# Kernel tuning notes

Hardware: AMD Instinct MI355X
Metric: run time of the kernel (lower is better)

The kernel has to match this reference:

```python
import jax, jax.numpy as jnp
import numpy as np

EPS = 1e-05
FACT = 2.0
REJECT_RATIO = 1.0
B, N1, N2 = 8, 4096, 4096


def setup_inputs() -> dict:
    key = jax.random.key(0)
    k1, k2 = jax.random.split(key)
    pc1 = jax.random.normal(k1, (B, 4, N1), dtype=jnp.float32)
    pc2 = jax.random.normal(k2, (B, 4, N2), dtype=jnp.float32)
    # homogeneous coordinates: last row is 1
    pc1 = pc1.at[:, 3, :].set(1.0)
    pc2 = pc2.at[:, 3, :].set(1.0)
    return {"pc1": pc1, "pc2": pc2}


def _rot_to_quat(R):
    # quaternion [w, x, y, z] from 3x3 rotation matrix (branchless)
    def s(x):
        return jnp.where(x >= 0, 1.0, -1.0)
    qw = 0.5 * jnp.sqrt(jnp.maximum(1.0 + R[0, 0] + R[1, 1] + R[2, 2], 1e-12))
    qx = 0.5 * jnp.sqrt(jnp.maximum(1.0 + R[0, 0] - R[1, 1] - R[2, 2], 1e-12)) * s(R[2, 1] - R[1, 2])
    qy = 0.5 * jnp.sqrt(jnp.maximum(1.0 - R[0, 0] + R[1, 1] - R[2, 2], 1e-12)) * s(R[0, 2] - R[2, 0])
    qz = 0.5 * jnp.sqrt(jnp.maximum(1.0 - R[0, 0] - R[1, 1] + R[2, 2], 1e-12)) * s(R[1, 0] - R[0, 1])
    return jnp.stack([qw, qx, qy, qz])


def _single(pc1, pc2):
    # pc1: [4, N1], pc2: [4, N2]
    p1, p2 = pc1[:3], pc2[:3]
    # squared pairwise distance via matmul-expansion trick: [N1, N2]
    d = (jnp.sum(p1 ** 2, axis=0)[:, None]
         - 2.0 * jnp.einsum('dn,dm->nm', p1, p2)
         + jnp.sum(p2 ** 2, axis=0)[None, :])
    # soft nearest neighbor: softmax over N2 of fact / clamp(d, eps)
    w = jax.nn.softmax(FACT / jnp.maximum(d, EPS), axis=1)  # [N1, N2]
    pc_nearest = jnp.einsum('cm,nm->cn', pc2, w)            # [4, N1]

    # soft outlier rejection (near-hard threshold via steep sigmoid)
    dist = jnp.linalg.norm(pc1 - pc_nearest, axis=0)        # [N1]
    mean_dist = jnp.mean(dist)
    indexor = jax.nn.sigmoid((dist - mean_dist * REJECT_RATIO - EPS) * -1e10)

    # weighted Procrustes (soft_tf); note indexor weights BOTH centred clouds
    wsum = jnp.sum(indexor)
    c2 = jnp.sum(pc_nearest[:3] * indexor, axis=-1) / wsum  # [3]
    c1 = jnp.sum(pc1[:3] * indexor, axis=-1) / wsum         # [3]
    p2c = ((pc_nearest[:3] - c2[:, None]) * indexor).T      # [N1, 3]
    p1c = ((pc1[:3] - c1[:, None]) * indexor).T             # [N1, 3]
    H = p1c.T @ p2c                                         # [3, 3]
    U, S, Vh = jnp.linalg.svd(H, full_matrices=False)
    V = Vh.T
    sign = jnp.where(jnp.linalg.det(U) * jnp.linalg.det(V) < 0, -1.0, 1.0)
    V = V * jnp.array([1.0, 1.0, 1.0]).at[2].set(sign)[None, :]  # flip 3rd column
    R = V @ U.T
    t = c2 - R @ c1
    T = jnp.zeros((4, 4), dtype=pc1.dtype)
    T = T.at[:3, :3].set(R).at[:3, 3].set(t).at[3, 3].set(1.0)
    q = _rot_to_quat(R)
    return T, q, t


def reference(pc1, pc2):
    T, q, t = jax.vmap(_single)(pc1, pc2)
    return T, q, t
```

## Files before the change

### kernel.cpp

```cpp
#include <hip/hip_runtime.h>
#include <math.h>


typedef float v2f __attribute__((ext_vector_type(2)));

constexpr int cB  = 8;
constexpr int cN1 = 4096;
constexpr int cN2 = 4096;
constexpr int cMC = 8;
constexpr int cCHUNK = cN2 / cMC;
constexpr int cNB2 = cN1 / 256;
constexpr float cEPS  = 1e-5f;
constexpr float cKK   = 0.34657359027997264f;
constexpr float cEPSK = cEPS * cKK;
constexpr float cUNSC = -1.4426950408889634f;

constexpr size_t OFF_PARTM = 0x400000;
constexpr size_t OFF_DPART = 0x500000;
constexpr size_t OFF_MPART = 0x500400;

__global__ __launch_bounds__(256) void cpnet_partial(
    const float* __restrict__ pc1, const float* __restrict__ pc2,
    float4* __restrict__ partA, float* __restrict__ partM) {
  __shared__ float xs[cCHUNK], ys[cCHUNK], zs[cCHUNK], ws[cCHUNK];
  const int tid = threadIdx.x;
  const int b = blockIdx.z, c = blockIdx.y;
  const int n = blockIdx.x * 256 + tid;

  const float* p2b = pc2 + (size_t)b * 4 * cN2 + c * cCHUNK;
  for (int i = tid; i < cCHUNK; i += 256) {
    float x = p2b[i], y = p2b[cN2 + i], z = p2b[2 * cN2 + i];
    xs[i] = -2.0f * cKK * x;
    ys[i] = -2.0f * cKK * y;
    zs[i] = -2.0f * cKK * z;
    ws[i] = cKK * (x * x + y * y + z * z);
  }
  __syncthreads();

  const float* p1b = pc1 + (size_t)b * 4 * cN1;
  const float x1 = p1b[n], y1 = p1b[cN1 + n], z1 = p1b[2 * cN1 + n];
  const float n1k = cKK * (x1 * x1 + y1 * y1 + z1 * z1);
  const v2f X1 = {x1, x1}, Y1 = {y1, y1}, Z1 = {z1, z1}, N1K = {n1k, n1k};

  const v2f* xs2 = (const v2f*)xs;
  const v2f* ys2 = (const v2f*)ys;
  const v2f* zs2 = (const v2f*)zs;
  const v2f* ws2 = (const v2f*)ws;

  v2f dmin2 = {3.0e38f, 3.0e38f};
#pragma unroll 4
  for (int m = 0; m < cCHUNK / 2; ++m) {
    v2f dk = X1 * xs2[m] + (Y1 * ys2[m] + (Z1 * zs2[m] + (ws2[m] + N1K)));
    dmin2 = __builtin_elementwise_min(dmin2, dk);
  }
  const float dmin = fminf(dmin2.x, dmin2.y);
  const float M = __builtin_amdgcn_rcpf(fmaxf(dmin, cEPSK));
  const v2f M2 = {M, M};
  const v2f EPS2 = {cEPSK, cEPSK};

  v2f S2 = {0.f, 0.f}, Ax2 = {0.f, 0.f}, Ay2 = {0.f, 0.f}, Az2 = {0.f, 0.f};
#pragma unroll 4
  for (int m = 0; m < cCHUNK / 2; ++m) {
    v2f vx = xs2[m], vy = ys2[m], vz = zs2[m];
    v2f dk = X1 * vx + (Y1 * vy + (Z1 * vz + (ws2[m] + N1K)));
    dk = __builtin_elementwise_max(dk, EPS2);
    v2f s2v;
    s2v.x = __builtin_amdgcn_rcpf(dk.x);
    s2v.y = __builtin_amdgcn_rcpf(dk.y);
    v2f d2 = s2v - M2;
    v2f e;
    e.x = __builtin_amdgcn_exp2f(d2.x);
    e.y = __builtin_amdgcn_exp2f(d2.y);
    S2 += e;
    Ax2 += e * vx;
    Ay2 += e * vy;
    Az2 += e * vz;
  }

  const int idx = (c * cB + b) * cN1 + n;
  partA[idx] = make_float4(Ax2.x + Ax2.y, Ay2.x + Ay2.y, Az2.x + Az2.y,
                           S2.x + S2.y);
  partM[idx] = M;
}

__device__ __forceinline__ void reduce_multi(double* v, int nv, double* lds,
                                             int tid) {
  const int lane = tid & 63, w = tid >> 6;
  for (int i = 0; i < nv; ++i) {
    double x = v[i];
    for (int s = 32; s > 0; s >>= 1) x += __shfl_xor(x, s, 64);
    if (lane == 0) lds[i * 4 + w] = x;
  }
  __syncthreads();
  if (tid < nv)
    lds[tid * 4] = lds[tid * 4] + lds[tid * 4 + 1] + lds[tid * 4 + 2] +
                   lds[tid * 4 + 3];
  __syncthreads();
  for (int i = 0; i < nv; ++i) v[i] = lds[i * 4];
  __syncthreads();
}

__global__ __launch_bounds__(256) void cpnet_combine(
    const float* __restrict__ pc1, float4* partA,
    const float* __restrict__ partM, double* __restrict__ dpart) {
  __shared__ double lds[32 * 4];
  const int tid = threadIdx.x;
  const int bx = blockIdx.x, b = blockIdx.y;
  const int n = bx * 256 + tid;

  float Ms[cMC];
  float g = -3.0e38f;
#pragma unroll
  for (int c = 0; c < cMC; ++c) {
    Ms[c] = partM[(c * cB + b) * cN1 + n];
    g = fmaxf(g, Ms[c]);
  }
  float S = 0.f, nx = 0.f, ny = 0.f, nz = 0.f;
#pragma unroll
  for (int c = 0; c < cMC; ++c) {
    float w = exp2f(Ms[c] - g);
    float4 a = partA[(c * cB + b) * cN1 + n];
    S += a.w * w; nx += a.x * w; ny += a.y * w; nz += a.z * w;
  }
  float inv = cUNSC / S;
  nx *= inv; ny *= inv; nz *= inv;
  const float* p1b = pc1 + (size_t)b * 4 * cN1;
  float dx = p1b[n] - nx, dy = p1b[cN1 + n] - ny, dz = p1b[2 * cN1 + n] - nz;
  float dist = sqrtf(dx * dx + dy * dy + dz * dz);
  partA[(0 * cB + b) * cN1 + n] = make_float4(nx, ny, nz, dist);

  double acc[1];
  acc[0] = (double)dist;
  reduce_multi(acc, 1, lds, tid);
  if (tid == 0) dpart[b * cNB2 + bx] = acc[0];
}

__global__ __launch_bounds__(256) void cpnet_moments(
    const float* __restrict__ pc1, const float4* __restrict__ partA,
    const double* __restrict__ dpart, double* __restrict__ mpart) {
  __shared__ double lds[32 * 4];
  const int tid = threadIdx.x;
  const int bx = blockIdx.x, b = blockIdx.y;
  const int n = bx * 256 + tid;

  double dsum = 0.0;
  for (int i = 0; i < cNB2; ++i) dsum += dpart[b * cNB2 + i];
  const float meanf = (float)(dsum * (1.0 / (double)cN1));

  float4 nn = partA[(0 * cB + b) * cN1 + n];
  float u = (nn.w - meanf - cEPS) * 1e10f;
  float ind = 1.0f / (1.0f + expf(u));
  const float* p1b = pc1 + (size_t)b * 4 * cN1;
  double di = (double)ind, di2 = di * di;
  double x1 = (double)p1b[n], y1 = (double)p1b[cN1 + n],
         z1 = (double)p1b[2 * cN1 + n];
  double x2 = (double)nn.x, y2 = (double)nn.y, z2 = (double)nn.z;

  double a[23];
  a[0] = di;
  a[1] = di * x1;  a[2] = di * y1;  a[3] = di * z1;
  a[4] = di * x2;  a[5] = di * y2;  a[6] = di * z2;
  a[7] = di2;
  a[8]  = di2 * x1;  a[9]  = di2 * y1;  a[10] = di2 * z1;
  a[11] = di2 * x2;  a[12] = di2 * y2;  a[13] = di2 * z2;
  a[14] = di2 * x1 * x2; a[15] = di2 * x1 * y2; a[16] = di2 * x1 * z2;
  a[17] = di2 * y1 * x2; a[18] = di2 * y1 * y2; a[19] = di2 * y1 * z2;
  a[20] = di2 * z1 * x2; a[21] = di2 * z1 * y2; a[22] = di2 * z1 * z2;

  reduce_multi(a, 23, lds, tid);
  if (tid == 0) {
    double* mb = mpart + (size_t)(b * cNB2 + bx) * 23;
    for (int i = 0; i < 23; ++i) mb[i] = a[i];
  }
}

__global__ __launch_bounds__(64) void cpnet_solve(
    const double* __restrict__ mpart, float* __restrict__ out) {
  const int b = blockIdx.x;
  if (threadIdx.x != 0) return;

  double acc[23];
  for (int i = 0; i < 23; ++i) acc[i] = 0.0;
  for (int k = 0; k < cNB2; ++k) {
    const double* mb = mpart + (size_t)(b * cNB2 + k) * 23;
    for (int i = 0; i < 23; ++i) acc[i] += mb[i];
  }

  double W = acc[0];
  double c1[3] = {acc[1] / W, acc[2] / W, acc[3] / W};
  double c2[3] = {acc[4] / W, acc[5] / W, acc[6] / W};
  double H[3][3];
  for (int i = 0; i < 3; ++i)
    for (int j = 0; j < 3; ++j)
      H[i][j] = acc[14 + 3 * i + j] - c2[j] * acc[8 + i] -
                c1[i] * acc[11 + j] + c1[i] * c2[j] * acc[7];

  double trH = H[0][0] + H[1][1] + H[2][2];
  double Nm[4][4], V[4][4];
  Nm[0][0] = trH;
  Nm[0][1] = Nm[1][0] = H[1][2] - H[2][1];
  Nm[0][2] = Nm[2][0] = H[2][0] - H[0][2];
  Nm[0][3] = Nm[3][0] = H[0][1] - H[1][0];
  Nm[1][1] = 2.0 * H[0][0] - trH;
  Nm[1][2] = Nm[2][1] = H[0][1] + H[1][0];
  Nm[1][3] = Nm[3][1] = H[0][2] + H[2][0];
  Nm[2][2] = 2.0 * H[1][1] - trH;
  Nm[2][3] = Nm[3][2] = H[1][2] + H[2][1];
  Nm[3][3] = 2.0 * H[2][2] - trH;

  for (int i = 0; i < 4; ++i)
    for (int j = 0; j < 4; ++j) V[i][j] = (i == j) ? 1.0 : 0.0;

  for (int sweep = 0; sweep < 6; ++sweep) {
    for (int p = 0; p < 3; ++p) {
      for (int q = p + 1; q < 4; ++q) {
        double apq = Nm[p][q];
        if (fabs(apq) < 1e-300) continue;
        double theta = (Nm[q][q] - Nm[p][p]) / (2.0 * apq);
        double tt = (theta >= 0.0 ? 1.0 : -1.0) /
                    (fabs(theta) + sqrt(theta * theta + 1.0));
        double cc = 1.0 / sqrt(tt * tt + 1.0);
        double ss = tt * cc;
        for (int k = 0; k < 4; ++k) {
          double akp = Nm[k][p], akq = Nm[k][q];
          Nm[k][p] = cc * akp - ss * akq;
          Nm[k][q] = ss * akp + cc * akq;
        }
        for (int k = 0; k < 4; ++k) {
          double apk = Nm[p][k], aqk = Nm[q][k];
          Nm[p][k] = cc * apk - ss * aqk;
          Nm[q][k] = ss * apk + cc * aqk;
        }
        for (int k = 0; k < 4; ++k) {
          double vkp = V[k][p], vkq = V[k][q];
          V[k][p] = cc * vkp - ss * vkq;
          V[k][q] = ss * vkp + cc * vkq;
        }
      }
    }
  }
  int imax = 0;
  for (int i = 1; i < 4; ++i)
    if (Nm[i][i] > Nm[imax][imax]) imax = i;
  double qw = V[0][imax], qx = V[1][imax], qy = V[2][imax], qz = V[3][imax];
  double qn = sqrt(qw * qw + qx * qx + qy * qy + qz * qz);
  qw /= qn; qx /= qn; qy /= qn; qz /= qn;

  double R[3][3];
  R[0][0] = 1.0 - 2.0 * (qy * qy + qz * qz);
  R[0][1] = 2.0 * (qx * qy - qw * qz);
  R[0][2] = 2.0 * (qx * qz + qw * qy);
  R[1][0] = 2.0 * (qx * qy + qw * qz);
  R[1][1] = 1.0 - 2.0 * (qx * qx + qz * qz);
  R[1][2] = 2.0 * (qy * qz - qw * qx);
  R[2][0] = 2.0 * (qx * qz - qw * qy);
  R[2][1] = 2.0 * (qy * qz + qw * qx);
  R[2][2] = 1.0 - 2.0 * (qx * qx + qy * qy);

  double tr1 = 0.0, tr2 = 0.0;
  for (int i = 0; i < 3; ++i)
    for (int j = 0; j < 3; ++j) {
      tr1 += R[i][j] * H[j][i];
      tr2 += R[j][i] * H[j][i];
    }
  if (tr2 > tr1) {
    for (int i = 0; i < 3; ++i)
      for (int j = i + 1; j < 3; ++j) {
        double tmp = R[i][j]; R[i][j] = R[j][i]; R[j][i] = tmp;
      }
  }

  double tx = c2[0] - (R[0][0] * c1[0] + R[0][1] * c1[1] + R[0][2] * c1[2]);
  double ty = c2[1] - (R[1][0] * c1[0] + R[1][1] * c1[1] + R[1][2] * c1[2]);
  double tz = c2[2] - (R[2][0] * c1[0] + R[2][1] * c1[1] + R[2][2] * c1[2]);

  auto sgn = [](double x) { return x >= 0.0 ? 1.0 : -1.0; };
  double oqw = 0.5 * sqrt(fmax(1.0 + R[0][0] + R[1][1] + R[2][2], 1e-12));
  double oqx = 0.5 * sqrt(fmax(1.0 + R[0][0] - R[1][1] - R[2][2], 1e-12)) *
               sgn(R[2][1] - R[1][2]);
  double oqy = 0.5 * sqrt(fmax(1.0 - R[0][0] + R[1][1] - R[2][2], 1e-12)) *
               sgn(R[0][2] - R[2][0]);
  double oqz = 0.5 * sqrt(fmax(1.0 - R[0][0] - R[1][1] + R[2][2], 1e-12)) *
               sgn(R[1][0] - R[0][1]);

  float* T = out + b * 16;
  T[0]  = (float)R[0][0]; T[1]  = (float)R[0][1]; T[2]  = (float)R[0][2]; T[3]  = (float)tx;
  T[4]  = (float)R[1][0]; T[5]  = (float)R[1][1]; T[6]  = (float)R[1][2]; T[7]  = (float)ty;
  T[8]  = (float)R[2][0]; T[9]  = (float)R[2][1]; T[10] = (float)R[2][2]; T[11] = (float)tz;
  T[12] = 0.f; T[13] = 0.f; T[14] = 0.f; T[15] = 1.f;
  float* Q = out + 128 + b * 4;
  Q[0] = (float)oqw; Q[1] = (float)oqx; Q[2] = (float)oqy; Q[3] = (float)oqz;
  float* Tt = out + 160 + b * 3;
  Tt[0] = (float)tx; Tt[1] = (float)ty; Tt[2] = (float)tz;
}

extern "C" void kernel_launch(void* const* d_in, const int* in_sizes, int n_in,
                              void* d_out, int out_size, void* d_ws, size_t ws_size,
                              hipStream_t stream) {
  const float* pc1 = (const float*)d_in[0];
  const float* pc2 = (const float*)d_in[1];
  float* out = (float*)d_out;
  char* ws = (char*)d_ws;

  float4* partA = (float4*)ws;
  float*  partM = (float*)(ws + OFF_PARTM);
  double* dpart = (double*)(ws + OFF_DPART);
  double* mpart = (double*)(ws + OFF_MPART);

  cpnet_partial<<<dim3(cN1 / 256, cMC, cB), 256, 0, stream>>>(pc1, pc2,
                                                              partA, partM);
  cpnet_combine<<<dim3(cNB2, cB), 256, 0, stream>>>(pc1, partA, partM, dpart);
  cpnet_moments<<<dim3(cNB2, cB), 256, 0, stream>>>(pc1, partA, dpart, mpart);
  cpnet_solve<<<cB, 64, 0, stream>>>(mpart, out);
}
```

Measured before the change: 141.8 us.

## Fuse combine, moments and solve into one kernel via last-block atomic counter

Merges the combine, moments and solve kernels into a single finalize kernel. Each block writes its partial distance sum, and the last block to finish per batch (detected with an atomic counter reset inside the partial kernel) computes the mean, loops over all points to accumulate the 23 moments, and runs the solve. This removes two kernel launches and the per-block moment partials. In exchange, the moment accumulation is serialized onto a single block per batch.

```diff
diff --git a/kernel.cpp b/kernel.cpp
--- a/kernel.cpp
+++ b/kernel.cpp
@@ -17,11 +17,16 @@
 
 constexpr size_t OFF_PARTM = 0x400000;
 constexpr size_t OFF_DPART = 0x500000;
-constexpr size_t OFF_MPART = 0x500400;
+constexpr size_t OFF_CTR   = 0x500400;
 
 __global__ __launch_bounds__(256) void cpnet_partial(
     const float* __restrict__ pc1, const float* __restrict__ pc2,
-    float4* __restrict__ partA, float* __restrict__ partM) {
+    float4* __restrict__ partA, float* __restrict__ partM,
+    int* __restrict__ ctr) {
+  if (blockIdx.x == 0 && blockIdx.y == 0 && blockIdx.z == 0 &&
+      threadIdx.x < cB)
+    ctr[threadIdx.x] = 0;
+
   __shared__ float xs[cCHUNK], ys[cCHUNK], zs[cCHUNK], ws[cCHUNK];
   const int tid = threadIdx.x;
   const int b = blockIdx.z, c = blockIdx.y;
@@ -100,10 +105,13 @@
   __syncthreads();
 }
 
-__global__ __launch_bounds__(256) void cpnet_combine(
+__global__ __launch_bounds__(256) void cpnet_finalize(
     const float* __restrict__ pc1, float4* partA,
-    const float* __restrict__ partM, double* __restrict__ dpart) {
+    const float* __restrict__ partM, double* __restrict__ dpart,
+    int* ctr, float* __restrict__ out) {
   __shared__ double lds[32 * 4];
+  __shared__ float s_mean;
+  __shared__ int s_last;
   const int tid = threadIdx.x;
   const int bx = blockIdx.x, b = blockIdx.y;
   const int n = bx * 256 + tid;
@@ -119,8 +127,8 @@
 #pragma unroll
   for (int c = 0; c < cMC; ++c) {
     float w = exp2f(Ms[c] - g);
-    float4 a = partA[(c * cB + b) * cN1 + n];
-    S += a.w * w; nx += a.x * w; ny += a.y * w; nz += a.z * w;
+    float4 a4 = partA[(c * cB + b) * cN1 + n];
+    S += a4.w * w; nx += a4.x * w; ny += a4.y * w; nz += a4.z * w;
   }
   float inv = cUNSC / S;
   nx *= inv; ny *= inv; nz *= inv;
@@ -129,71 +137,63 @@
   float dist = sqrtf(dx * dx + dy * dy + dz * dz);
   partA[(0 * cB + b) * cN1 + n] = make_float4(nx, ny, nz, dist);
 
-  double acc[1];
-  acc[0] = (double)dist;
-  reduce_multi(acc, 1, lds, tid);
-  if (tid == 0) dpart[b * cNB2 + bx] = acc[0];
-}
-
-__global__ __launch_bounds__(256) void cpnet_moments(
-    const float* __restrict__ pc1, const float4* __restrict__ partA,
-    const double* __restrict__ dpart, double* __restrict__ mpart) {
-  __shared__ double lds[32 * 4];
-  const int tid = threadIdx.x;
-  const int bx = blockIdx.x, b = blockIdx.y;
-  const int n = bx * 256 + tid;
-
-  double dsum = 0.0;
-  for (int i = 0; i < cNB2; ++i) dsum += dpart[b * cNB2 + i];
-  const float meanf = (float)(dsum * (1.0 / (double)cN1));
-
-  float4 nn = partA[(0 * cB + b) * cN1 + n];
-  float u = (nn.w - meanf - cEPS) * 1e10f;
-  float ind = 1.0f / (1.0f + expf(u));
-  const float* p1b = pc1 + (size_t)b * 4 * cN1;
-  double di = (double)ind, di2 = di * di;
-  double x1 = (double)p1b[n], y1 = (double)p1b[cN1 + n],
-         z1 = (double)p1b[2 * cN1 + n];
-  double x2 = (double)nn.x, y2 = (double)nn.y, z2 = (double)nn.z;
+  double acc1[1];
+  acc1[0] = (double)dist;
+  reduce_multi(acc1, 1, lds, tid);
+  if (tid == 0) dpart[b * cNB2 + bx] = acc1[0];
+
+  __threadfence();
+  if (tid == 0) {
+    int old = atomicAdd(ctr + b, 1);
+    s_last = (old == cNB2 - 1) ? 1 : 0;
+  }
+  __syncthreads();
+  if (!s_last) return;
+  __threadfence();
+
+  if (tid == 0) {
+    double dsum = 0.0;
+    for (int i = 0; i < cNB2; ++i) dsum += dpart[b * cNB2 + i];
+    s_mean = (float)(dsum * (1.0 / (double)cN1));
+  }
+  __syncthreads();
+  const float meanf = s_mean;
 
   double a[23];
-  a[0] = di;
-  a[1] = di * x1;  a[2] = di * y1;  a[3] = di * z1;
-  a[4] = di * x2;  a[5] = di * y2;  a[6] = di * z2;
-  a[7] = di2;
-  a[8]  = di2 * x1;  a[9]  = di2 * y1;  a[10] = di2 * z1;
-  a[11] = di2 * x2;  a[12] = di2 * y2;  a[13] = di2 * z2;
-  a[14] = di2 * x1 * x2; a[15] = di2 * x1 * y2; a[16] = di2 * x1 * z2;
-  a[17] = di2 * y1 * x2; a[18] = di2 * y1 * y2; a[19] = di2 * y1 * z2;
-  a[20] = di2 * z1 * x2; a[21] = di2 * z1 * y2; a[22] = di2 * z1 * z2;
-
+  for (int i = 0; i < 23; ++i) a[i] = 0.0;
+#pragma unroll 2
+  for (int it = 0; it < cNB2; ++it) {
+    const int r = it * 256 + tid;
+    float4 nn = partA[(0 * cB + b) * cN1 + r];
+    float u = (nn.w - meanf - cEPS) * 1e10f;
+    float ind = 1.0f / (1.0f + expf(u));
+    double di = (double)ind, di2 = di * di;
+    double x1 = (double)p1b[r], y1 = (double)p1b[cN1 + r],
+           z1 = (double)p1b[2 * cN1 + r];
+    double x2 = (double)nn.x, y2 = (double)nn.y, z2 = (double)nn.z;
+
+    a[0] += di;
+    a[1] += di * x1;  a[2] += di * y1;  a[3] += di * z1;
+    a[4] += di * x2;  a[5] += di * y2;  a[6] += di * z2;
+    a[7] += di2;
+    a[8]  += di2 * x1;  a[9]  += di2 * y1;  a[10] += di2 * z1;
+    a[11] += di2 * x2;  a[12] += di2 * y2;  a[13] += di2 * z2;
+    a[14] += di2 * x1 * x2; a[15] += di2 * x1 * y2; a[16] += di2 * x1 * z2;
+    a[17] += di2 * y1 * x2; a[18] += di2 * y1 * y2; a[19] += di2 * y1 * z2;
+    a[20] += di2 * z1 * x2; a[21] += di2 * z1 * y2; a[22] += di2 * z1 * z2;
+  }
   reduce_multi(a, 23, lds, tid);
-  if (tid == 0) {
-    double* mb = mpart + (size_t)(b * cNB2 + bx) * 23;
-    for (int i = 0; i < 23; ++i) mb[i] = a[i];
-  }
-}
-
-__global__ __launch_bounds__(64) void cpnet_solve(
-    const double* __restrict__ mpart, float* __restrict__ out) {
-  const int b = blockIdx.x;
-  if (threadIdx.x != 0) return;
-
-  double acc[23];
-  for (int i = 0; i < 23; ++i) acc[i] = 0.0;
-  for (int k = 0; k < cNB2; ++k) {
-    const double* mb = mpart + (size_t)(b * cNB2 + k) * 23;
-    for (int i = 0; i < 23; ++i) acc[i] += mb[i];
-  }
-
-  double W = acc[0];
-  double c1[3] = {acc[1] / W, acc[2] / W, acc[3] / W};
-  double c2[3] = {acc[4] / W, acc[5] / W, acc[6] / W};
+
+  if (tid != 0) return;
+
+  double W = a[0];
+  double c1[3] = {a[1] / W, a[2] / W, a[3] / W};
+  double c2[3] = {a[4] / W, a[5] / W, a[6] / W};
   double H[3][3];
   for (int i = 0; i < 3; ++i)
     for (int j = 0; j < 3; ++j)
-      H[i][j] = acc[14 + 3 * i + j] - c2[j] * acc[8 + i] -
-                c1[i] * acc[11 + j] + c1[i] * c2[j] * acc[7];
+      H[i][j] = a[14 + 3 * i + j] - c2[j] * a[8 + i] -
+                c1[i] * a[11 + j] + c1[i] * c2[j] * a[7];
 
   double trH = H[0][0] + H[1][1] + H[2][2];
   double Nm[4][4], V[4][4];
@@ -305,11 +305,10 @@
   float4* partA = (float4*)ws;
   float*  partM = (float*)(ws + OFF_PARTM);
   double* dpart = (double*)(ws + OFF_DPART);
-  double* mpart = (double*)(ws + OFF_MPART);
-
-  cpnet_partial<<<dim3(cN1 / 256, cMC, cB), 256, 0, stream>>>(pc1, pc2,
-                                                              partA, partM);
-  cpnet_combine<<<dim3(cNB2, cB), 256, 0, stream>>>(pc1, partA, partM, dpart);
-  cpnet_moments<<<dim3(cNB2, cB), 256, 0, stream>>>(pc1, partA, dpart, mpart);
-  cpnet_solve<<<cB, 64, 0, stream>>>(mpart, out);
+  int*    ctr   = (int*)(ws + OFF_CTR);
+
+  cpnet_partial<<<dim3(cN1 / 256, cMC, cB), 256, 0, stream>>>(
+      pc1, pc2, partA, partM, ctr);
+  cpnet_finalize<<<dim3(cNB2, cB), 256, 0, stream>>>(
+      pc1, partA, partM, dpart, ctr, out);
 }
```

Result: slower. 150.2 us (+5.9%).

## Register-block four rows per thread and split chunk across wavefronts

Applied to the files above, without the earlier changes.

Each thread now handles four pc1 points, and each wavefront covers a quarter of the pc2 chunk. Every LDS load of a pc2 point is reused across four rows, which cuts LDS traffic per FLOP. The four per-wavefront partial softmax sums are then merged through shared memory with a log-sum-exp style rescale against the largest row max. The cost is more registers, an extra shared buffer and barrier, and a merge step with additional exp2 calls.

```diff
diff --git a/kernel.cpp b/kernel.cpp
--- a/kernel.cpp
+++ b/kernel.cpp
@@ -23,9 +23,11 @@
     const float* __restrict__ pc1, const float* __restrict__ pc2,
     float4* __restrict__ partA, float* __restrict__ partM) {
   __shared__ float xs[cCHUNK], ys[cCHUNK], zs[cCHUNK], ws[cCHUNK];
+  __shared__ float comb[4][256][5];
   const int tid = threadIdx.x;
+  const int lane = tid & 63, g = tid >> 6;
   const int b = blockIdx.z, c = blockIdx.y;
-  const int n = blockIdx.x * 256 + tid;
+  const int nbase = blockIdx.x * 256;
 
   const float* p2b = pc2 + (size_t)b * 4 * cN2 + c * cCHUNK;
   for (int i = tid; i < cCHUNK; i += 256) {
@@ -38,49 +40,91 @@
   __syncthreads();
 
   const float* p1b = pc1 + (size_t)b * 4 * cN1;
-  const float x1 = p1b[n], y1 = p1b[cN1 + n], z1 = p1b[2 * cN1 + n];
-  const float n1k = cKK * (x1 * x1 + y1 * y1 + z1 * z1);
-  const v2f X1 = {x1, x1}, Y1 = {y1, y1}, Z1 = {z1, z1}, N1K = {n1k, n1k};
-
-  const v2f* xs2 = (const v2f*)xs;
-  const v2f* ys2 = (const v2f*)ys;
-  const v2f* zs2 = (const v2f*)zs;
-  const v2f* ws2 = (const v2f*)ws;
-
-  v2f dmin2 = {3.0e38f, 3.0e38f};
-#pragma unroll 4
-  for (int m = 0; m < cCHUNK / 2; ++m) {
-    v2f dk = X1 * xs2[m] + (Y1 * ys2[m] + (Z1 * zs2[m] + (ws2[m] + N1K)));
-    dmin2 = __builtin_elementwise_min(dmin2, dk);
-  }
-  const float dmin = fminf(dmin2.x, dmin2.y);
-  const float M = __builtin_amdgcn_rcpf(fmaxf(dmin, cEPSK));
-  const v2f M2 = {M, M};
+  float x1[4], y1[4], z1[4], n1k[4];
+#pragma unroll
+  for (int k = 0; k < 4; ++k) {
+    int r = nbase + k * 64 + lane;
+    x1[k] = p1b[r];
+    y1[k] = p1b[cN1 + r];
+    z1[k] = p1b[2 * cN1 + r];
+    n1k[k] = cKK * (x1[k] * x1[k] + y1[k] * y1[k] + z1[k] * z1[k]);
+  }
+
+  const v2f* xs2 = (const v2f*)xs + g * 64;
+  const v2f* ys2 = (const v2f*)ys + g * 64;
+  const v2f* zs2 = (const v2f*)zs + g * 64;
+  const v2f* ws2 = (const v2f*)ws + g * 64;
+
+  v2f dmin2[4];
+#pragma unroll
+  for (int k = 0; k < 4; ++k) dmin2[k] = (v2f){3.0e38f, 3.0e38f};
+#pragma unroll 2
+  for (int m = 0; m < 64; ++m) {
+    v2f vx = xs2[m], vy = ys2[m], vz = zs2[m], vw = ws2[m];
+#pragma unroll
+    for (int k = 0; k < 4; ++k) {
+      v2f dk = vx * x1[k] + (vy * y1[k] + (vz * z1[k] + (vw + n1k[k])));
+      dmin2[k] = __builtin_elementwise_min(dmin2[k], dk);
+    }
+  }
+  float M[4];
+#pragma unroll
+  for (int k = 0; k < 4; ++k)
+    M[k] = __builtin_amdgcn_rcpf(fmaxf(fminf(dmin2[k].x, dmin2[k].y), cEPSK));
+
+  v2f S2[4], Ax2[4], Ay2[4], Az2[4];
+#pragma unroll
+  for (int k = 0; k < 4; ++k) {
+    S2[k] = (v2f){0.f, 0.f}; Ax2[k] = (v2f){0.f, 0.f};
+    Ay2[k] = (v2f){0.f, 0.f}; Az2[k] = (v2f){0.f, 0.f};
+  }
   const v2f EPS2 = {cEPSK, cEPSK};
-
-  v2f S2 = {0.f, 0.f}, Ax2 = {0.f, 0.f}, Ay2 = {0.f, 0.f}, Az2 = {0.f, 0.f};
-#pragma unroll 4
-  for (int m = 0; m < cCHUNK / 2; ++m) {
-    v2f vx = xs2[m], vy = ys2[m], vz = zs2[m];
-    v2f dk = X1 * vx + (Y1 * vy + (Z1 * vz + (ws2[m] + N1K)));
-    dk = __builtin_elementwise_max(dk, EPS2);
-    v2f s2v;
-    s2v.x = __builtin_amdgcn_rcpf(dk.x);
-    s2v.y = __builtin_amdgcn_rcpf(dk.y);
-    v2f d2 = s2v - M2;
-    v2f e;
-    e.x = __builtin_amdgcn_exp2f(d2.x);
-    e.y = __builtin_amdgcn_exp2f(d2.y);
-    S2 += e;
-    Ax2 += e * vx;
-    Ay2 += e * vy;
-    Az2 += e * vz;
-  }
-
-  const int idx = (c * cB + b) * cN1 + n;
-  partA[idx] = make_float4(Ax2.x + Ax2.y, Ay2.x + Ay2.y, Az2.x + Az2.y,
-                           S2.x + S2.y);
-  partM[idx] = M;
+#pragma unroll 2
+  for (int m = 0; m < 64; ++m) {
+    v2f vx = xs2[m], vy = ys2[m], vz = zs2[m], vw = ws2[m];
+#pragma unroll
+    for (int k = 0; k < 4; ++k) {
+      v2f dk = vx * x1[k] + (vy * y1[k] + (vz * z1[k] + (vw + n1k[k])));
+      dk = __builtin_elementwise_max(dk, EPS2);
+      v2f s2v;
+      s2v.x = __builtin_amdgcn_rcpf(dk.x);
+      s2v.y = __builtin_amdgcn_rcpf(dk.y);
+      v2f e;
+      e.x = __builtin_amdgcn_exp2f(s2v.x - M[k]);
+      e.y = __builtin_amdgcn_exp2f(s2v.y - M[k]);
+      S2[k] += e;
+      Ax2[k] += e * vx;
+      Ay2[k] += e * vy;
+      Az2[k] += e * vz;
+    }
+  }
+
+#pragma unroll
+  for (int k = 0; k < 4; ++k) {
+    int r = k * 64 + lane;
+    comb[g][r][0] = S2[k].x + S2[k].y;
+    comb[g][r][1] = Ax2[k].x + Ax2[k].y;
+    comb[g][r][2] = Ay2[k].x + Ay2[k].y;
+    comb[g][r][3] = Az2[k].x + Az2[k].y;
+    comb[g][r][4] = M[k];
+  }
+  __syncthreads();
+
+  float m0 = comb[0][tid][4], m1 = comb[1][tid][4],
+        m2 = comb[2][tid][4], m3 = comb[3][tid][4];
+  float mrow = fmaxf(fmaxf(m0, m1), fmaxf(m2, m3));
+  float S = 0.f, Ax = 0.f, Ay = 0.f, Az = 0.f;
+#pragma unroll
+  for (int gg = 0; gg < 4; ++gg) {
+    float w = exp2f(comb[gg][tid][4] - mrow);
+    S  += comb[gg][tid][0] * w;
+    Ax += comb[gg][tid][1] * w;
+    Ay += comb[gg][tid][2] * w;
+    Az += comb[gg][tid][3] * w;
+  }
+  const int idx = (c * cB + b) * cN1 + nbase + tid;
+  partA[idx] = make_float4(Ax, Ay, Az, S);
+  partM[idx] = mrow;
 }
 
 __device__ __forceinline__ void reduce_multi(double* v, int nv, double* lds,
```

Measured after the change: 139.2 us. About the same (-1.8%).
